# Optimization experiments

Hardware: AMD Instinct MI355X
Metric: run time of the kernel (lower is better)

Reference implementation:

```python
import jax, jax.numpy as jnp
import numpy as np

N_NODES = 50000
N_EDGES = 800000
IN_FEATS = 128
H_FEATS = 128
OUT_FEATS = 64


def _mean_agg(h, src, dst, n_nodes):
    # mean over in-neighbors: sum h[src] into dst, divide by in-degree (0 for isolated nodes)
    summed = jax.ops.segment_sum(h[src], dst, num_segments=n_nodes)  # [N, d]
    deg = jax.ops.segment_sum(jnp.ones((src.shape[0],), h.dtype), dst, num_segments=n_nodes)
    return summed / jnp.maximum(deg, 1.0)[:, None]


def setup_inputs() -> dict:
    key = jax.random.key(0)
    ks = jax.random.split(key, 10)
    s = 0.05
    return {
        "inputs": jax.random.normal(ks[0], (N_NODES, IN_FEATS), jnp.float32),
        "fc_W": jax.random.normal(ks[1], (H_FEATS, IN_FEATS), jnp.float32) * s,
        "fc_b": jax.random.normal(ks[2], (H_FEATS,), jnp.float32) * s,
        "W": jax.random.normal(ks[3], (3, H_FEATS, H_FEATS), jnp.float32) * s,
        "b": jax.random.normal(ks[4], (3, H_FEATS), jnp.float32) * s,
        "W_last": jax.random.normal(ks[5], (OUT_FEATS, H_FEATS), jnp.float32) * s,
        "b_last": jax.random.normal(ks[6], (OUT_FEATS,), jnp.float32) * s,
        "eps": jnp.zeros((4,), jnp.float32),
        "src": jax.random.randint(ks[7], (N_EDGES,), 0, N_NODES, jnp.int32),
        "dst": jax.random.randint(ks[8], (N_EDGES,), 0, N_NODES, jnp.int32),
    }


def reference(inputs, fc_W, fc_b, W, b, W_last, b_last, eps, src, dst):
    n = inputs.shape[0]
    # input SLP
    h = jax.nn.relu(inputs @ fc_W.T + fc_b)
    # 3 hidden GIN layers: relu(Linear((1+eps)*h + mean_agg(h)))  (dropout = eval identity)
    for i in range(3):
        agg = _mean_agg(h, src, dst, n)
        h = jax.nn.relu(((1.0 + eps[i]) * h + agg) @ W[i].T + b[i])
    # last GIN layer (no ReLU)
    agg = _mean_agg(h, src, dst, n)
    h = ((1.0 + eps[3]) * h + agg) @ W_last.T + b_last
    return h
```

## Files before the change

### kernel.cpp

```cpp
#include <hip/hip_runtime.h>

#define N_NODES 50000
#define N_EDGES 800000
#define NBUCK 196
#define EPB 8192
#define NSTRIPE ((N_EDGES + EPB - 1) / EPB)

typedef __attribute__((ext_vector_type(8))) short short8;
typedef __attribute__((ext_vector_type(4))) float float4v;

__device__ inline unsigned short f2bf(float f) {
    unsigned u = __float_as_uint(f);
    unsigned r = u + 0x7fff + ((u >> 16) & 1);
    return (unsigned short)(r >> 16);
}
__device__ inline float bf2f(unsigned short h) {
    return __uint_as_float(((unsigned)h) << 16);
}


__global__ void __launch_bounds__(256) fused_hist_prep(
    const int* __restrict__ dst, int* __restrict__ bcnt, const float* __restrict__ fcW,
    const float* __restrict__ W, const float* __restrict__ Wl, unsigned short* __restrict__ hi,
    unsigned short* __restrict__ lo) {
    int bx = blockIdx.x;
    if (bx < NSTRIPE) {
        __shared__ int lhist[256];
        int t = threadIdx.x;
        lhist[t] = 0;
        __syncthreads();
        int base = bx * EPB + t;
#pragma unroll 4
        for (int k = 0; k < EPB / 256; k++) {
            int i = base + k * 256;
            if (i < N_EDGES) atomicAdd(&lhist[((unsigned)dst[i]) >> 8], 1);
        }
        __syncthreads();
        if (t < NBUCK) atomicAdd(&bcnt[t], lhist[t]);
    } else {
        int i = (bx - NSTRIPE) * 256 + threadIdx.x;
        float v;
        if (i < 16384) v = fcW[i];
        else if (i < 65536) v = W[i - 16384];
        else if (i < 73728) v = Wl[i - 65536];
        else return;
        unsigned short h = f2bf(v);
        hi[i] = h;
        lo[i] = f2bf(v - bf2f(h));
    }
}


__global__ void bucket_scan(const int* __restrict__ bcnt, int* __restrict__ boff,
                            int* __restrict__ cursor, int* __restrict__ row_ptr) {
    __shared__ int sm[256];
    int t = threadIdx.x;
    int v = (t < NBUCK) ? bcnt[t] : 0;
    sm[t] = v;
    __syncthreads();
    for (int o = 1; o < 256; o <<= 1) {
        int x = sm[t];
        int a = (t >= o) ? sm[t - o] : 0;
        __syncthreads();
        sm[t] = x + a;
        __syncthreads();
    }
    if (t < NBUCK) {
        boff[t] = sm[t] - v;
        cursor[t] = sm[t] - v;
    }
    if (t == NBUCK - 1) {
        boff[NBUCK] = sm[t];
        row_ptr[N_NODES] = sm[t];
    }
}


template <int COLS, bool RELU, bool WRITE_BF>
__device__ __forceinline__ void gemm_body(int bx, const float* __restrict__ U,
                                          const unsigned short* __restrict__ Whi,
                                          const unsigned short* __restrict__ Wlo,
                                          const float* __restrict__ bias, float* __restrict__ out,
                                          unsigned short* __restrict__ outbf, int nrows) {
    int wave = threadIdx.x >> 6;
    int lane = threadIdx.x & 63;
    int m = lane & 15;
    int quad = lane >> 4;
    int r0 = bx * 64 + wave * 16;
    int rowA = r0 + m;
    if (rowA >= nrows) rowA = nrows - 1;

    short8 ahi[4], alo[4];
    const float* arow = U + (size_t)rowA * 128 + quad * 8;
#pragma unroll
    for (int kc = 0; kc < 4; kc++) {
        float4 f0 = *(const float4*)(arow + kc * 32);
        float4 f1 = *(const float4*)(arow + kc * 32 + 4);
        float fv[8] = {f0.x, f0.y, f0.z, f0.w, f1.x, f1.y, f1.z, f1.w};
#pragma unroll
        for (int j = 0; j < 8; j++) {
            unsigned short h = f2bf(fv[j]);
            ahi[kc][j] = (short)h;
            alo[kc][j] = (short)f2bf(fv[j] - bf2f(h));
        }
    }

#pragma unroll
    for (int nt = 0; nt < COLS / 16; nt++) {
        int n = nt * 16 + m;
        const unsigned short* bhp = Whi + (size_t)n * 128 + quad * 8;
        const unsigned short* blp = Wlo + (size_t)n * 128 + quad * 8;
        float4v acc = {0.f, 0.f, 0.f, 0.f};
#pragma unroll
        for (int kc = 0; kc < 4; kc++) {
            short8 bh = *(const short8*)(bhp + kc * 32);
            short8 bl = *(const short8*)(blp + kc * 32);
            acc = __builtin_amdgcn_mfma_f32_16x16x32_bf16(ahi[kc], bh, acc, 0, 0, 0);
            acc = __builtin_amdgcn_mfma_f32_16x16x32_bf16(alo[kc], bh, acc, 0, 0, 0);
            acc = __builtin_amdgcn_mfma_f32_16x16x32_bf16(ahi[kc], bl, acc, 0, 0, 0);
        }
        float bv = bias[n];
#pragma unroll
        for (int i = 0; i < 4; i++) {
            int r = r0 + quad * 4 + i;
            if (r < nrows) {
                float v = acc[i] + bv;
                if (RELU) v = fmaxf(v, 0.f);
                out[(size_t)r * COLS + n] = v;
                if (WRITE_BF) outbf[(size_t)r * COLS + n] = f2bf(v);
            }
        }
    }
}

template <int COLS, bool RELU, bool WRITE_BF>
__global__ void __launch_bounds__(256) gemm_mfma(const float* __restrict__ U,
                                                 const unsigned short* __restrict__ Whi,
                                                 const unsigned short* __restrict__ Wlo,
                                                 const float* __restrict__ bias,
                                                 float* __restrict__ out,
                                                 unsigned short* __restrict__ outbf, int nrows) {
    gemm_body<COLS, RELU, WRITE_BF>(blockIdx.x, U, Whi, Wlo, bias, out, outbf, nrows);
}


__global__ void __launch_bounds__(256) fused_binA_gemm(
    const int* __restrict__ src, const int* __restrict__ dst, int* __restrict__ cursor,
    int* __restrict__ packed, const float* __restrict__ X, const unsigned short* __restrict__ whi,
    const unsigned short* __restrict__ wlo, const float* __restrict__ fcb, float* __restrict__ h,
    unsigned short* __restrict__ hbf) {
    int bx = blockIdx.x;
    if (bx < NSTRIPE) {
        __shared__ int lcount[256];
        __shared__ int lbase[256];
        int t = threadIdx.x;
        lcount[t] = 0;
        __syncthreads();
        int base = bx * EPB + t;
#pragma unroll 4
        for (int k = 0; k < EPB / 256; k++) {
            int i = base + k * 256;
            if (i < N_EDGES) atomicAdd(&lcount[((unsigned)dst[i]) >> 8], 1);
        }
        __syncthreads();
        if (t < NBUCK) {
            lbase[t] = atomicAdd(&cursor[t], lcount[t]);
            lcount[t] = 0;
        }
        __syncthreads();
#pragma unroll 4
        for (int k = 0; k < EPB / 256; k++) {
            int i = base + k * 256;
            if (i < N_EDGES) {
                int d = dst[i];
                int wb = ((unsigned)d) >> 8;
                int p = lbase[wb] + atomicAdd(&lcount[wb], 1);
                packed[p] = ((d & 255) << 16) | src[i];
            }
        }
    } else {
        gemm_body<128, true, true>(bx - NSTRIPE, X, whi, wlo, fcb, h, hbf, N_NODES);
    }
}


__global__ void __launch_bounds__(256) binB_kernel(const int* __restrict__ packed,
                                                   const int* __restrict__ boff,
                                                   int* __restrict__ row_ptr,
                                                   int* __restrict__ esrc) {
    __shared__ int sm[256];
    __shared__ int curs[256];
    int b = blockIdx.x;
    int t = threadIdx.x;
    int e0 = boff[b], e1 = boff[b + 1];
    curs[t] = 0;
    __syncthreads();
    for (int i = e0 + t; i < e1; i += 256) atomicAdd(&curs[((unsigned)packed[i]) >> 16], 1);
    __syncthreads();
    int v = curs[t];
    sm[t] = v;
    __syncthreads();
    for (int o = 1; o < 256; o <<= 1) {
        int x = sm[t];
        int a = (t >= o) ? sm[t - o] : 0;
        __syncthreads();
        sm[t] = x + a;
        __syncthreads();
    }
    int excl = sm[t] - v;
    curs[t] = excl;
    int node = b * 256 + t;
    if (node < N_NODES) row_ptr[node] = e0 + excl;
    __syncthreads();
    for (int i = e0 + t; i < e1; i += 256) {
        unsigned w = (unsigned)packed[i];
        int p = atomicAdd(&curs[w >> 16], 1);
        esrc[e0 + p] = (int)(w & 0xFFFFu);
    }
}


__global__ void agg_kernel(const float* __restrict__ h, const unsigned short* __restrict__ hbf,
                           const int* __restrict__ row_ptr, const int* __restrict__ esrc,
                           const float* __restrict__ eps, int layer, float* __restrict__ u) {
    int gtid = blockIdx.x * 256 + threadIdx.x;
    int node = gtid >> 6;
    int lane = threadIdx.x & 63;
    if (node >= N_NODES) return;
    node = __builtin_amdgcn_readfirstlane(node);
    int beg = __builtin_amdgcn_readfirstlane(row_ptr[node]);
    int end = __builtin_amdgcn_readfirstlane(row_ptr[node + 1]);

    const unsigned short* hl = hbf + lane * 2;
    float a0x = 0.f, a0y = 0.f, a1x = 0.f, a1y = 0.f;
    float a2x = 0.f, a2y = 0.f, a3x = 0.f, a3y = 0.f;
    int e = beg;
    for (; e + 3 < end; e += 4) {
        int s0 = esrc[e], s1 = esrc[e + 1], s2 = esrc[e + 2], s3 = esrc[e + 3];
        unsigned v0 = *(const unsigned*)(hl + (size_t)s0 * 128);
        unsigned v1 = *(const unsigned*)(hl + (size_t)s1 * 128);
        unsigned v2 = *(const unsigned*)(hl + (size_t)s2 * 128);
        unsigned v3 = *(const unsigned*)(hl + (size_t)s3 * 128);
        a0x += bf2f((unsigned short)v0); a0y += bf2f((unsigned short)(v0 >> 16));
        a1x += bf2f((unsigned short)v1); a1y += bf2f((unsigned short)(v1 >> 16));
        a2x += bf2f((unsigned short)v2); a2y += bf2f((unsigned short)(v2 >> 16));
        a3x += bf2f((unsigned short)v3); a3y += bf2f((unsigned short)(v3 >> 16));
    }
    for (; e < end; e++) {
        int s = esrc[e];
        unsigned v = *(const unsigned*)(hl + (size_t)s * 128);
        a0x += bf2f((unsigned short)v);
        a0y += bf2f((unsigned short)(v >> 16));
    }
    float sx = (a0x + a1x) + (a2x + a3x);
    float sy = (a0y + a1y) + (a2y + a3y);
    int d = end - beg;
    float inv = (d > 0) ? 1.0f / (float)d : 0.0f;
    float ep = 1.0f + eps[layer];
    float2 hv = *(const float2*)(h + (size_t)node * 128 + lane * 2);
    float2 r;
    r.x = ep * hv.x + sx * inv;
    r.y = ep * hv.y + sy * inv;
    *(float2*)(u + (size_t)node * 128 + lane * 2) = r;
}


extern "C" void kernel_launch(void* const* d_in, const int* in_sizes, int n_in,
                              void* d_out, int out_size, void* d_ws, size_t ws_size,
                              hipStream_t stream) {
    const float* X   = (const float*)d_in[0];
    const float* fcW = (const float*)d_in[1];
    const float* fcb = (const float*)d_in[2];
    const float* W   = (const float*)d_in[3];
    const float* b   = (const float*)d_in[4];
    const float* Wl  = (const float*)d_in[5];
    const float* bl  = (const float*)d_in[6];
    const float* eps = (const float*)d_in[7];
    const int* src   = (const int*)d_in[8];
    const int* dst   = (const int*)d_in[9];
    float* out = (float*)d_out;

    float* h = (float*)d_ws;
    float* u = h + (size_t)N_NODES * 128;
    unsigned short* hbf = (unsigned short*)(u + (size_t)N_NODES * 128);
    unsigned short* whi = hbf + (size_t)N_NODES * 128;
    unsigned short* wlo = whi + 73728;
    int* bcnt    = (int*)(wlo + 73728);
    int* boff    = bcnt + NBUCK;
    int* cursor  = boff + NBUCK + 1;
    int* row_ptr = cursor + NBUCK;
    int* packed  = row_ptr + N_NODES + 1;
    int* esrc    = packed + N_EDGES;

    const int gemm_blocks = (N_NODES + 63) / 64;
    const int agg_blocks = (N_NODES * 64 + 255) / 256;
    const int prep_blocks = (73728 + 255) / 256;

    hipMemsetAsync(bcnt, 0, NBUCK * sizeof(int), stream);
    fused_hist_prep<<<NSTRIPE + prep_blocks, 256, 0, stream>>>(dst, bcnt, fcW, W, Wl, whi, wlo);
    bucket_scan<<<1, 256, 0, stream>>>(bcnt, boff, cursor, row_ptr);
    fused_binA_gemm<<<NSTRIPE + gemm_blocks, 256, 0, stream>>>(src, dst, cursor, packed, X, whi,
                                                               wlo, fcb, h, hbf);
    binB_kernel<<<NBUCK, 256, 0, stream>>>(packed, boff, row_ptr, esrc);

    for (int i = 0; i < 3; i++) {
        agg_kernel<<<agg_blocks, 256, 0, stream>>>(h, hbf, row_ptr, esrc, eps, i, u);
        gemm_mfma<128, true, true><<<gemm_blocks, 256, 0, stream>>>(
            u, whi + 16384 + (size_t)i * 16384, wlo + 16384 + (size_t)i * 16384,
            b + (size_t)i * 128, h, hbf, N_NODES);
    }

    agg_kernel<<<agg_blocks, 256, 0, stream>>>(h, hbf, row_ptr, esrc, eps, 3, u);
    gemm_mfma<64, false, false><<<gemm_blocks, 256, 0, stream>>>(u, whi + 65536, wlo + 65536, bl,
                                                                 out, nullptr, N_NODES);
}
```

Before: 431.0 us.

## Fuse aggregation into GEMM via LDS and reorder last layer as project-then-aggregate

Each hidden layer now aggregates neighbors and applies the linear layer in one kernel. The aggregated rows are split into bf16 hi/lo parts and stored in swizzled LDS, so the fp32 intermediate u no longer makes a round trip through global memory. The last layer exploits linearity: it first projects h to 64 features, then aggregates the narrower rows and adds the bias, halving the gather width. It also halves edges-per-block in binning and ping-pongs bf16 buffers, at the cost of lower aggregation parallelism per block (each wave handles 16 nodes serially) and extra rounding from the reordering.

```diff
diff --git a/kernel.cpp b/kernel.cpp
--- a/kernel.cpp
+++ b/kernel.cpp
@@ -3,7 +3,7 @@
 #define N_NODES 50000
 #define N_EDGES 800000
 #define NBUCK 196
-#define EPB 8192
+#define EPB 4096
 #define NSTRIPE ((N_EDGES + EPB - 1) / EPB)
 
 typedef __attribute__((ext_vector_type(8))) short short8;
@@ -76,7 +76,7 @@
 }
 
 
-template <int COLS, bool RELU, bool WRITE_BF>
+template <int COLS, bool RELU, bool WRITE_BF, bool BIAS>
 __device__ __forceinline__ void gemm_body(int bx, const float* __restrict__ U,
                                           const unsigned short* __restrict__ Whi,
                                           const unsigned short* __restrict__ Wlo,
@@ -119,7 +119,8 @@
             acc = __builtin_amdgcn_mfma_f32_16x16x32_bf16(alo[kc], bh, acc, 0, 0, 0);
             acc = __builtin_amdgcn_mfma_f32_16x16x32_bf16(ahi[kc], bl, acc, 0, 0, 0);
         }
-        float bv = bias[n];
+        float bv = 0.f;
+        if (BIAS) bv = bias[n];
 #pragma unroll
         for (int i = 0; i < 4; i++) {
             int r = r0 + quad * 4 + i;
@@ -133,14 +134,14 @@
     }
 }
 
-template <int COLS, bool RELU, bool WRITE_BF>
+template <int COLS, bool RELU, bool WRITE_BF, bool BIAS>
 __global__ void __launch_bounds__(256) gemm_mfma(const float* __restrict__ U,
                                                  const unsigned short* __restrict__ Whi,
                                                  const unsigned short* __restrict__ Wlo,
                                                  const float* __restrict__ bias,
                                                  float* __restrict__ out,
                                                  unsigned short* __restrict__ outbf, int nrows) {
-    gemm_body<COLS, RELU, WRITE_BF>(blockIdx.x, U, Whi, Wlo, bias, out, outbf, nrows);
+    gemm_body<COLS, RELU, WRITE_BF, BIAS>(blockIdx.x, U, Whi, Wlo, bias, out, outbf, nrows);
 }
 
 
@@ -179,7 +180,7 @@
             }
         }
     } else {
-        gemm_body<128, true, true>(bx - NSTRIPE, X, whi, wlo, fcb, h, hbf, N_NODES);
+        gemm_body<128, true, true, true>(bx - NSTRIPE, X, whi, wlo, fcb, h, hbf, N_NODES);
     }
 }
 
@@ -220,48 +221,145 @@
 }
 
 
-__global__ void agg_kernel(const float* __restrict__ h, const unsigned short* __restrict__ hbf,
-                           const int* __restrict__ row_ptr, const int* __restrict__ esrc,
-                           const float* __restrict__ eps, int layer, float* __restrict__ u) {
+template <bool WRITE_BF>
+__global__ void __launch_bounds__(256) fused_agg_gemm(
+    float* __restrict__ hio, const unsigned short* __restrict__ bfin,
+    const int* __restrict__ row_ptr, const int* __restrict__ esrc,
+    const float* __restrict__ eps, int layer, const unsigned short* __restrict__ Whi,
+    const unsigned short* __restrict__ Wlo, const float* __restrict__ bias,
+    unsigned short* __restrict__ bfout) {
+    __shared__ unsigned lds_hi[4096];
+    __shared__ unsigned lds_lo[4096];
+    int tid = threadIdx.x;
+    int wv = tid >> 6;
+    int lane = tid & 63;
+    int r0 = blockIdx.x * 64;
+    unsigned basew = (unsigned)(wv << 10);
+    float ep = 1.0f + eps[layer];
+    const unsigned short* hl = bfin + lane * 2;
+
+    for (int i = 0; i < 16; i++) {
+        int node = r0 + wv * 16 + i;
+        if (node >= N_NODES) break;
+        int beg = __builtin_amdgcn_readfirstlane(row_ptr[node]);
+        int end = __builtin_amdgcn_readfirstlane(row_ptr[node + 1]);
+        float a0x = 0.f, a0y = 0.f, a1x = 0.f, a1y = 0.f;
+        float a2x = 0.f, a2y = 0.f, a3x = 0.f, a3y = 0.f;
+        int e = beg;
+        for (; e + 3 < end; e += 4) {
+            int s0 = esrc[e], s1 = esrc[e + 1], s2 = esrc[e + 2], s3 = esrc[e + 3];
+            unsigned v0 = *(const unsigned*)(hl + (size_t)s0 * 128);
+            unsigned v1 = *(const unsigned*)(hl + (size_t)s1 * 128);
+            unsigned v2 = *(const unsigned*)(hl + (size_t)s2 * 128);
+            unsigned v3 = *(const unsigned*)(hl + (size_t)s3 * 128);
+            a0x += bf2f((unsigned short)v0); a0y += bf2f((unsigned short)(v0 >> 16));
+            a1x += bf2f((unsigned short)v1); a1y += bf2f((unsigned short)(v1 >> 16));
+            a2x += bf2f((unsigned short)v2); a2y += bf2f((unsigned short)(v2 >> 16));
+            a3x += bf2f((unsigned short)v3); a3y += bf2f((unsigned short)(v3 >> 16));
+        }
+        for (; e < end; e++) {
+            int s = esrc[e];
+            unsigned v = *(const unsigned*)(hl + (size_t)s * 128);
+            a0x += bf2f((unsigned short)v);
+            a0y += bf2f((unsigned short)(v >> 16));
+        }
+        float sx = (a0x + a1x) + (a2x + a3x);
+        float sy = (a0y + a1y) + (a2y + a3y);
+        int d = end - beg;
+        float inv = (d > 0) ? 1.0f / (float)d : 0.0f;
+        float2 hv = *(const float2*)(hio + (size_t)node * 128 + lane * 2);
+        float ux = ep * hv.x + sx * inv;
+        float uy = ep * hv.y + sy * inv;
+        unsigned short u0 = f2bf(ux), u1 = f2bf(uy);
+        unsigned hi = (unsigned)u0 | ((unsigned)u1 << 16);
+        unsigned lo = (unsigned)f2bf(ux - bf2f(u0)) | ((unsigned)f2bf(uy - bf2f(u1)) << 16);
+        unsigned idx = basew + (unsigned)(i * 64) + (unsigned)(lane ^ ((i & 7) << 2));
+        lds_hi[idx] = hi;
+        lds_lo[idx] = lo;
+    }
+    __syncthreads();
+
+    int m = lane & 15, quad = lane >> 4;
+    short8 ahi[4], alo[4];
+#pragma unroll
+    for (int kc = 0; kc < 4; kc++) {
+        unsigned idx =
+            basew + (unsigned)(m * 64) + (unsigned)((kc * 16 + quad * 4) ^ ((m & 7) << 2));
+        ahi[kc] = *(const short8*)&lds_hi[idx];
+        alo[kc] = *(const short8*)&lds_lo[idx];
+    }
+    int rbase = r0 + wv * 16;
+#pragma unroll
+    for (int nt = 0; nt < 8; nt++) {
+        int n = nt * 16 + m;
+        const unsigned short* bhp = Whi + (size_t)n * 128 + quad * 8;
+        const unsigned short* blp = Wlo + (size_t)n * 128 + quad * 8;
+        float4v acc = {0.f, 0.f, 0.f, 0.f};
+#pragma unroll
+        for (int kc = 0; kc < 4; kc++) {
+            short8 bh = *(const short8*)(bhp + kc * 32);
+            short8 bl2 = *(const short8*)(blp + kc * 32);
+            acc = __builtin_amdgcn_mfma_f32_16x16x32_bf16(ahi[kc], bh, acc, 0, 0, 0);
+            acc = __builtin_amdgcn_mfma_f32_16x16x32_bf16(alo[kc], bh, acc, 0, 0, 0);
+            acc = __builtin_amdgcn_mfma_f32_16x16x32_bf16(ahi[kc], bl2, acc, 0, 0, 0);
+        }
+        float bv = bias[n];
+#pragma unroll
+        for (int i2 = 0; i2 < 4; i2++) {
+            int r = rbase + quad * 4 + i2;
+            if (r < N_NODES) {
+                float v = fmaxf(acc[i2] + bv, 0.f);
+                hio[(size_t)r * 128 + n] = v;
+                if (WRITE_BF) bfout[(size_t)r * 128 + n] = f2bf(v);
+            }
+        }
+    }
+}
+
+
+__global__ void __launch_bounds__(256) agg64_out(
+    const float* __restrict__ g, const unsigned short* __restrict__ gbf,
+    const int* __restrict__ row_ptr, const int* __restrict__ esrc,
+    const float* __restrict__ eps, const float* __restrict__ bl, float* __restrict__ out) {
     int gtid = blockIdx.x * 256 + threadIdx.x;
     int node = gtid >> 6;
+    if (node >= N_NODES) return;
     int lane = threadIdx.x & 63;
-    if (node >= N_NODES) return;
     node = __builtin_amdgcn_readfirstlane(node);
     int beg = __builtin_amdgcn_readfirstlane(row_ptr[node]);
     int end = __builtin_amdgcn_readfirstlane(row_ptr[node + 1]);
-
-    const unsigned short* hl = hbf + lane * 2;
-    float a0x = 0.f, a0y = 0.f, a1x = 0.f, a1y = 0.f;
-    float a2x = 0.f, a2y = 0.f, a3x = 0.f, a3y = 0.f;
-    int e = beg;
-    for (; e + 3 < end; e += 4) {
-        int s0 = esrc[e], s1 = esrc[e + 1], s2 = esrc[e + 2], s3 = esrc[e + 3];
-        unsigned v0 = *(const unsigned*)(hl + (size_t)s0 * 128);
-        unsigned v1 = *(const unsigned*)(hl + (size_t)s1 * 128);
-        unsigned v2 = *(const unsigned*)(hl + (size_t)s2 * 128);
-        unsigned v3 = *(const unsigned*)(hl + (size_t)s3 * 128);
-        a0x += bf2f((unsigned short)v0); a0y += bf2f((unsigned short)(v0 >> 16));
-        a1x += bf2f((unsigned short)v1); a1y += bf2f((unsigned short)(v1 >> 16));
-        a2x += bf2f((unsigned short)v2); a2y += bf2f((unsigned short)(v2 >> 16));
-        a3x += bf2f((unsigned short)v3); a3y += bf2f((unsigned short)(v3 >> 16));
-    }
-    for (; e < end; e++) {
+    int half = lane >> 5;
+    int fp = lane & 31;
+    const unsigned short* gl = gbf + fp * 2;
+    float ax = 0.f, ay = 0.f, bx = 0.f, by = 0.f;
+    int e = beg + half;
+    for (; e + 2 < end; e += 4) {
+        int s0 = esrc[e], s1 = esrc[e + 2];
+        unsigned v0 = *(const unsigned*)(gl + (size_t)s0 * 64);
+        unsigned v1 = *(const unsigned*)(gl + (size_t)s1 * 64);
+        ax += bf2f((unsigned short)v0); ay += bf2f((unsigned short)(v0 >> 16));
+        bx += bf2f((unsigned short)v1); by += bf2f((unsigned short)(v1 >> 16));
+    }
+    for (; e < end; e += 2) {
         int s = esrc[e];
-        unsigned v = *(const unsigned*)(hl + (size_t)s * 128);
-        a0x += bf2f((unsigned short)v);
-        a0y += bf2f((unsigned short)(v >> 16));
-    }
-    float sx = (a0x + a1x) + (a2x + a3x);
-    float sy = (a0y + a1y) + (a2y + a3y);
-    int d = end - beg;
-    float inv = (d > 0) ? 1.0f / (float)d : 0.0f;
-    float ep = 1.0f + eps[layer];
-    float2 hv = *(const float2*)(h + (size_t)node * 128 + lane * 2);
-    float2 r;
-    r.x = ep * hv.x + sx * inv;
-    r.y = ep * hv.y + sy * inv;
-    *(float2*)(u + (size_t)node * 128 + lane * 2) = r;
+        unsigned v = *(const unsigned*)(gl + (size_t)s * 64);
+        ax += bf2f((unsigned short)v);
+        ay += bf2f((unsigned short)(v >> 16));
+    }
+    ax += bx;
+    ay += by;
+    ax += __shfl_xor(ax, 32);
+    ay += __shfl_xor(ay, 32);
+    if (half == 0) {
+        int d = end - beg;
+        float inv = (d > 0) ? 1.0f / (float)d : 0.0f;
+        float ep = 1.0f + eps[3];
+        float2 gv = *(const float2*)(g + (size_t)node * 64 + fp * 2);
+        float2 r;
+        r.x = ep * gv.x + ax * inv + bl[fp * 2];
+        r.y = ep * gv.y + ay * inv + bl[fp * 2 + 1];
+        *(float2*)(out + (size_t)node * 64 + fp * 2) = r;
+    }
 }
 
 
@@ -281,9 +379,9 @@
     float* out = (float*)d_out;
 
     float* h = (float*)d_ws;
-    float* u = h + (size_t)N_NODES * 128;
-    unsigned short* hbf = (unsigned short*)(u + (size_t)N_NODES * 128);
-    unsigned short* whi = hbf + (size_t)N_NODES * 128;
+    unsigned short* bfA = (unsigned short*)(h + (size_t)N_NODES * 128);
+    unsigned short* bfB = bfA + (size_t)N_NODES * 128;
+    unsigned short* whi = bfB + (size_t)N_NODES * 128;
     unsigned short* wlo = whi + 73728;
     int* bcnt    = (int*)(wlo + 73728);
     int* boff    = bcnt + NBUCK;
@@ -291,26 +389,29 @@
     int* row_ptr = cursor + NBUCK;
     int* packed  = row_ptr + N_NODES + 1;
     int* esrc    = packed + N_EDGES;
+    float* g = (float*)bfB;
+    unsigned short* gbf = bfA;
 
     const int gemm_blocks = (N_NODES + 63) / 64;
-    const int agg_blocks = (N_NODES * 64 + 255) / 256;
+    const int agg64_blocks = (N_NODES * 64 + 255) / 256;
     const int prep_blocks = (73728 + 255) / 256;
 
     hipMemsetAsync(bcnt, 0, NBUCK * sizeof(int), stream);
     fused_hist_prep<<<NSTRIPE + prep_blocks, 256, 0, stream>>>(dst, bcnt, fcW, W, Wl, whi, wlo);
     bucket_scan<<<1, 256, 0, stream>>>(bcnt, boff, cursor, row_ptr);
     fused_binA_gemm<<<NSTRIPE + gemm_blocks, 256, 0, stream>>>(src, dst, cursor, packed, X, whi,
-                                                               wlo, fcb, h, hbf);
+                                                               wlo, fcb, h, bfA);
     binB_kernel<<<NBUCK, 256, 0, stream>>>(packed, boff, row_ptr, esrc);
 
-    for (int i = 0; i < 3; i++) {
-        agg_kernel<<<agg_blocks, 256, 0, stream>>>(h, hbf, row_ptr, esrc, eps, i, u);
-        gemm_mfma<128, true, true><<<gemm_blocks, 256, 0, stream>>>(
-            u, whi + 16384 + (size_t)i * 16384, wlo + 16384 + (size_t)i * 16384,
-            b + (size_t)i * 128, h, hbf, N_NODES);
-    }
-
-    agg_kernel<<<agg_blocks, 256, 0, stream>>>(h, hbf, row_ptr, esrc, eps, 3, u);
-    gemm_mfma<64, false, false><<<gemm_blocks, 256, 0, stream>>>(u, whi + 65536, wlo + 65536, bl,
-                                                                 out, nullptr, N_NODES);
-}
+    fused_agg_gemm<true><<<gemm_blocks, 256, 0, stream>>>(h, bfA, row_ptr, esrc, eps, 0,
+                                                          whi + 16384, wlo + 16384, b, bfB);
+    fused_agg_gemm<true><<<gemm_blocks, 256, 0, stream>>>(h, bfB, row_ptr, esrc, eps, 1,
+                                                          whi + 32768, wlo + 32768, b + 128, bfA);
+    fused_agg_gemm<false><<<gemm_blocks, 256, 0, stream>>>(h, bfA, row_ptr, esrc, eps, 2,
+                                                           whi + 49152, wlo + 49152, b + 256, bfB);
+
+    gemm_mfma<64, false, true, false><<<gemm_blocks, 256, 0, stream>>>(h, whi + 65536,
+                                                                       wlo + 65536, nullptr, g,
+                                                                       gbf, N_NODES);
+    agg64_out<<<agg64_blocks, 256, 0, stream>>>(g, gbf, row_ptr, esrc, eps, bl, out);
+}
```

Result: slower. 456.3 us (+5.9%).

## Reorder last GIN layer to project before aggregating and pre-split bf16 activations

Applied to the files above, without the earlier changes.

The final layer now applies the 128-to-64 linear map first and then mean-aggregates the 64-wide result, adding the bias afterwards. This uses linearity to halve the gather traffic of the last aggregation. The aggregation kernel now writes pre-split bf16 hi/lo operands, so the GEMM no longer reads fp32 inputs and splits them itself. The binning stripe size is also halved for more parallelism. The reordering changes floating-point summation order slightly, and the last aggregation now gathers bf16-rounded projected values.

```diff
diff --git a/kernel.cpp b/kernel.cpp
--- a/kernel.cpp
+++ b/kernel.cpp
@@ -3,7 +3,7 @@
 #define N_NODES 50000
 #define N_EDGES 800000
 #define NBUCK 196
-#define EPB 8192
+#define EPB 4096
 #define NSTRIPE ((N_EDGES + EPB - 1) / EPB)
 
 typedef __attribute__((ext_vector_type(8))) short short8;
@@ -76,8 +76,10 @@
 }
 
 
-template <int COLS, bool RELU, bool WRITE_BF>
+template <int COLS, bool RELU, bool WRITE_BF, bool BIAS, bool ASPLIT>
 __device__ __forceinline__ void gemm_body(int bx, const float* __restrict__ U,
+                                          const unsigned short* __restrict__ Uhi,
+                                          const unsigned short* __restrict__ Ulo,
                                           const unsigned short* __restrict__ Whi,
                                           const unsigned short* __restrict__ Wlo,
                                           const float* __restrict__ bias, float* __restrict__ out,
@@ -91,17 +93,27 @@
     if (rowA >= nrows) rowA = nrows - 1;
 
     short8 ahi[4], alo[4];
-    const float* arow = U + (size_t)rowA * 128 + quad * 8;
-#pragma unroll
-    for (int kc = 0; kc < 4; kc++) {
-        float4 f0 = *(const float4*)(arow + kc * 32);
-        float4 f1 = *(const float4*)(arow + kc * 32 + 4);
-        float fv[8] = {f0.x, f0.y, f0.z, f0.w, f1.x, f1.y, f1.z, f1.w};
-#pragma unroll
-        for (int j = 0; j < 8; j++) {
-            unsigned short h = f2bf(fv[j]);
-            ahi[kc][j] = (short)h;
-            alo[kc][j] = (short)f2bf(fv[j] - bf2f(h));
+    if (ASPLIT) {
+        const unsigned short* hp = Uhi + (size_t)rowA * 128 + quad * 8;
+        const unsigned short* lp = Ulo + (size_t)rowA * 128 + quad * 8;
+#pragma unroll
+        for (int kc = 0; kc < 4; kc++) {
+            ahi[kc] = *(const short8*)(hp + kc * 32);
+            alo[kc] = *(const short8*)(lp + kc * 32);
+        }
+    } else {
+        const float* arow = U + (size_t)rowA * 128 + quad * 8;
+#pragma unroll
+        for (int kc = 0; kc < 4; kc++) {
+            float4 f0 = *(const float4*)(arow + kc * 32);
+            float4 f1 = *(const float4*)(arow + kc * 32 + 4);
+            float fv[8] = {f0.x, f0.y, f0.z, f0.w, f1.x, f1.y, f1.z, f1.w};
+#pragma unroll
+            for (int j = 0; j < 8; j++) {
+                unsigned short h = f2bf(fv[j]);
+                ahi[kc][j] = (short)h;
+                alo[kc][j] = (short)f2bf(fv[j] - bf2f(h));
+            }
         }
     }
 
@@ -119,7 +131,8 @@
             acc = __builtin_amdgcn_mfma_f32_16x16x32_bf16(alo[kc], bh, acc, 0, 0, 0);
             acc = __builtin_amdgcn_mfma_f32_16x16x32_bf16(ahi[kc], bl, acc, 0, 0, 0);
         }
-        float bv = bias[n];
+        float bv = 0.f;
+        if (BIAS) bv = bias[n];
 #pragma unroll
         for (int i = 0; i < 4; i++) {
             int r = r0 + quad * 4 + i;
@@ -133,14 +146,17 @@
     }
 }
 
-template <int COLS, bool RELU, bool WRITE_BF>
+template <int COLS, bool RELU, bool WRITE_BF, bool BIAS, bool ASPLIT>
 __global__ void __launch_bounds__(256) gemm_mfma(const float* __restrict__ U,
+                                                 const unsigned short* __restrict__ Uhi,
+                                                 const unsigned short* __restrict__ Ulo,
                                                  const unsigned short* __restrict__ Whi,
                                                  const unsigned short* __restrict__ Wlo,
                                                  const float* __restrict__ bias,
                                                  float* __restrict__ out,
                                                  unsigned short* __restrict__ outbf, int nrows) {
-    gemm_body<COLS, RELU, WRITE_BF>(blockIdx.x, U, Whi, Wlo, bias, out, outbf, nrows);
+    gemm_body<COLS, RELU, WRITE_BF, BIAS, ASPLIT>(blockIdx.x, U, Uhi, Ulo, Whi, Wlo, bias, out,
+                                                  outbf, nrows);
 }
 
 
@@ -179,7 +195,8 @@
             }
         }
     } else {
-        gemm_body<128, true, true>(bx - NSTRIPE, X, whi, wlo, fcb, h, hbf, N_NODES);
+        gemm_body<128, true, true, true, false>(bx - NSTRIPE, X, nullptr, nullptr, whi, wlo, fcb,
+                                                h, hbf, N_NODES);
     }
 }
 
@@ -220,9 +237,11 @@
 }
 
 
-__global__ void agg_kernel(const float* __restrict__ h, const unsigned short* __restrict__ hbf,
-                           const int* __restrict__ row_ptr, const int* __restrict__ esrc,
-                           const float* __restrict__ eps, int layer, float* __restrict__ u) {
+__global__ void __launch_bounds__(256) agg_kernel(
+    const float* __restrict__ h, const unsigned short* __restrict__ hbf,
+    const int* __restrict__ row_ptr, const int* __restrict__ esrc,
+    const float* __restrict__ eps, int layer, unsigned* __restrict__ uhi32,
+    unsigned* __restrict__ ulo32) {
     int gtid = blockIdx.x * 256 + threadIdx.x;
     int node = gtid >> 6;
     int lane = threadIdx.x & 63;
@@ -258,10 +277,58 @@
     float inv = (d > 0) ? 1.0f / (float)d : 0.0f;
     float ep = 1.0f + eps[layer];
     float2 hv = *(const float2*)(h + (size_t)node * 128 + lane * 2);
-    float2 r;
-    r.x = ep * hv.x + sx * inv;
-    r.y = ep * hv.y + sy * inv;
-    *(float2*)(u + (size_t)node * 128 + lane * 2) = r;
+    float ux = ep * hv.x + sx * inv;
+    float uy = ep * hv.y + sy * inv;
+    unsigned short u0 = f2bf(ux), u1 = f2bf(uy);
+    size_t o = (size_t)node * 64 + lane;
+    uhi32[o] = (unsigned)u0 | ((unsigned)u1 << 16);
+    ulo32[o] = (unsigned)f2bf(ux - bf2f(u0)) | ((unsigned)f2bf(uy - bf2f(u1)) << 16);
+}
+
+
+__global__ void __launch_bounds__(256) agg64_out(
+    const float* __restrict__ g, const unsigned short* __restrict__ gbf,
+    const int* __restrict__ row_ptr, const int* __restrict__ esrc,
+    const float* __restrict__ eps, const float* __restrict__ bl, float* __restrict__ out) {
+    int gtid = blockIdx.x * 256 + threadIdx.x;
+    int node = gtid >> 6;
+    if (node >= N_NODES) return;
+    int lane = threadIdx.x & 63;
+    node = __builtin_amdgcn_readfirstlane(node);
+    int beg = __builtin_amdgcn_readfirstlane(row_ptr[node]);
+    int end = __builtin_amdgcn_readfirstlane(row_ptr[node + 1]);
+    int half = lane >> 5;
+    int fp = lane & 31;
+    const unsigned short* gl = gbf + fp * 2;
+    float ax = 0.f, ay = 0.f, bx = 0.f, by = 0.f;
+    int e = beg + half;
+    for (; e + 2 < end; e += 4) {
+        int s0 = esrc[e], s1 = esrc[e + 2];
+        unsigned v0 = *(const unsigned*)(gl + (size_t)s0 * 64);
+        unsigned v1 = *(const unsigned*)(gl + (size_t)s1 * 64);
+        ax += bf2f((unsigned short)v0); ay += bf2f((unsigned short)(v0 >> 16));
+        bx += bf2f((unsigned short)v1); by += bf2f((unsigned short)(v1 >> 16));
+    }
+    for (; e < end; e += 2) {
+        int s = esrc[e];
+        unsigned v = *(const unsigned*)(gl + (size_t)s * 64);
+        ax += bf2f((unsigned short)v);
+        ay += bf2f((unsigned short)(v >> 16));
+    }
+    ax += bx;
+    ay += by;
+    ax += __shfl_xor(ax, 32);
+    ay += __shfl_xor(ay, 32);
+    if (half == 0) {
+        int d = end - beg;
+        float inv = (d > 0) ? 1.0f / (float)d : 0.0f;
+        float ep = 1.0f + eps[3];
+        float2 gv = *(const float2*)(g + (size_t)node * 64 + fp * 2);
+        float2 r;
+        r.x = ep * gv.x + ax * inv + bl[fp * 2];
+        r.y = ep * gv.y + ay * inv + bl[fp * 2 + 1];
+        *(float2*)(out + (size_t)node * 64 + fp * 2) = r;
+    }
 }
 
 
@@ -281,9 +348,10 @@
     float* out = (float*)d_out;
 
     float* h = (float*)d_ws;
-    float* u = h + (size_t)N_NODES * 128;
-    unsigned short* hbf = (unsigned short*)(u + (size_t)N_NODES * 128);
-    unsigned short* whi = hbf + (size_t)N_NODES * 128;
+    unsigned short* hbf = (unsigned short*)(h + (size_t)N_NODES * 128);
+    unsigned short* uhi = hbf + (size_t)N_NODES * 128;
+    unsigned short* ulo = uhi + (size_t)N_NODES * 128;
+    unsigned short* whi = ulo + (size_t)N_NODES * 128;
     unsigned short* wlo = whi + 73728;
     int* bcnt    = (int*)(wlo + 73728);
     int* boff    = bcnt + NBUCK;
@@ -291,6 +359,8 @@
     int* row_ptr = cursor + NBUCK;
     int* packed  = row_ptr + N_NODES + 1;
     int* esrc    = packed + N_EDGES;
+    float* g = (float*)uhi;
+    unsigned short* gbf = ulo;
 
     const int gemm_blocks = (N_NODES + 63) / 64;
     const int agg_blocks = (N_NODES * 64 + 255) / 256;
@@ -304,13 +374,19 @@
     binB_kernel<<<NBUCK, 256, 0, stream>>>(packed, boff, row_ptr, esrc);
 
     for (int i = 0; i < 3; i++) {
-        agg_kernel<<<agg_blocks, 256, 0, stream>>>(h, hbf, row_ptr, esrc, eps, i, u);
-        gemm_mfma<128, true, true><<<gemm_blocks, 256, 0, stream>>>(
-            u, whi + 16384 + (size_t)i * 16384, wlo + 16384 + (size_t)i * 16384,
-            b + (size_t)i * 128, h, hbf, N_NODES);
-    }
-
-    agg_kernel<<<agg_blocks, 256, 0, stream>>>(h, hbf, row_ptr, esrc, eps, 3, u);
-    gemm_mfma<64, false, false><<<gemm_blocks, 256, 0, stream>>>(u, whi + 65536, wlo + 65536, bl,
-                                                                 out, nullptr, N_NODES);
-}
+        agg_kernel<<<agg_blocks, 256, 0, stream>>>(h, hbf, row_ptr, esrc, eps, i,
+                                                   (unsigned*)uhi, (unsigned*)ulo);
+        if (i < 2)
+            gemm_mfma<128, true, true, true, true><<<gemm_blocks, 256, 0, stream>>>(
+                nullptr, uhi, ulo, whi + 16384 + (size_t)i * 16384,
+                wlo + 16384 + (size_t)i * 16384, b + (size_t)i * 128, h, hbf, N_NODES);
+        else
+            gemm_mfma<128, true, false, true, true><<<gemm_blocks, 256, 0, stream>>>(
+                nullptr, uhi, ulo, whi + 16384 + (size_t)i * 16384,
+                wlo + 16384 + (size_t)i * 16384, b + (size_t)i * 128, h, nullptr, N_NODES);
+    }
+
+    gemm_mfma<64, false, true, false, false><<<gemm_blocks, 256, 0, stream>>>(
+        h, nullptr, nullptr, whi + 65536, wlo + 65536, nullptr, g, gbf, N_NODES);
+    agg64_out<<<agg_blocks, 256, 0, stream>>>(g, gbf, row_ptr, esrc, eps, bl, out);
+}
```

Result: faster. 421.2 us (-2.3%).
